# Performance work log

Hardware: AMD Instinct MI355X
Metric: run time of the kernel (lower is better)

The kernel has to match this reference:

```python
import jax, jax.numpy as jnp
import numpy as np

NUM_BUCKETS = 63  # clipped 1D relative positions: clip(j-i, -31, 31) + 31


def _rp_bucket(N):
    rel = jnp.arange(N)[None, :] - jnp.arange(N)[:, None]  # j - i
    half = NUM_BUCKETS // 2
    return (jnp.clip(rel, -half, half) + half).astype(jnp.int32)  # [N, N]


def setup_inputs() -> dict:
    key = jax.random.key(0)
    ks = jax.random.split(key, 7)
    B, N, C, H = 4, 1024, 1024, 16
    hd = C // H
    g = lambda k, shp, sc: jax.random.normal(k, shp, jnp.float32) * sc
    return {
        "x": g(ks[0], (B, N, C), 1.0),
        "w_qkv": g(ks[1], (3 * C, C), C ** -0.5),   # torch Linear weight [out, in]
        "w_proj": g(ks[2], (C, C), C ** -0.5),
        "b_proj": jnp.zeros((C,), jnp.float32),
        "rpe_q_table": g(ks[3], (H, hd, NUM_BUCKETS), 0.02),
        "rpe_k_table": g(ks[4], (H, hd, NUM_BUCKETS), 0.02),
        "rpe_v_table": g(ks[5], (H, NUM_BUCKETS, hd), 0.02),
    }


def reference(x, w_qkv, w_proj, b_proj, rpe_q_table, rpe_k_table, rpe_v_table):
    B, N, C = x.shape
    H = rpe_k_table.shape[0]
    hd = C // H
    scale = hd ** -0.5

    qkv = (x @ w_qkv.T).reshape(B, N, 3, H, hd).transpose(2, 0, 3, 1, 4)  # [3,B,H,N,hd]
    q, k, v = qkv[0] * scale, qkv[1], qkv[2]

    attn = jnp.einsum('bhid,bhjd->bhij', q, k)  # [B,H,N,N]

    rp = _rp_bucket(N)            # [N,N] int32 (static w.r.t. jit)
    idx = rp[None, None]          # [1,1,N,N]

    # rpe_k(q): contextual product, transposed=True -> bias added to scores
    qL = jnp.einsum('bhid,hdm->bhim', q, rpe_k_table)           # [B,H,N,nb]
    attn = attn + jnp.take_along_axis(qL, idx, axis=-1)

    # rpe_q(k * scale).transpose(2,3)
    kL = jnp.einsum('bhjd,hdm->bhjm', k * scale, rpe_q_table)   # [B,H,N,nb]
    attn = attn + jnp.swapaxes(jnp.take_along_axis(kL, idx, axis=-1), 2, 3)

    attn = jax.nn.softmax(attn, axis=-1)

    out = jnp.einsum('bhij,bhjd->bhid', attn, v)  # [B,H,N,hd]

    # rpe_v(attn): out[b,h,i,d] += sum_j attn[b,h,i,j] * Lv[h, rp[i,j], d]
    # segment-sum attn over buckets per query row, then contract with table.
    a_t = attn.transpose(2, 3, 0, 1)  # [Ni, Nj, B, H]
    S = jax.vmap(lambda a, seg: jax.ops.segment_sum(a, seg, num_segments=NUM_BUCKETS))(a_t, rp)  # [Ni,nb,B,H]
    out = out + jnp.einsum('inbh,hnd->bhid', S, rpe_v_table)

    x_out = out.transpose(0, 2, 1, 3).reshape(B, N, C)
    return x_out @ w_proj.T + b_proj
```

## Files before the change

### kernel.cpp

```cpp
#include <hip/hip_runtime.h>

typedef unsigned short u16;
typedef __attribute__((ext_vector_type(8))) short bf16x8;
typedef __attribute__((ext_vector_type(8))) unsigned short u16x8;
typedef __attribute__((ext_vector_type(4))) float f32x4;

#define MFMA16(a, b, c) __builtin_amdgcn_mfma_f32_16x16x32_bf16(a, b, c, 0, 0, 0)

__device__ __forceinline__ u16 f2bf(float f) {
  union { float f; unsigned u; } v; v.f = f;
  unsigned r = v.u + 0x7fffu + ((v.u >> 16) & 1u);
  return (u16)(r >> 16);
}
__device__ __forceinline__ float bf2f(u16 h) {
  union { unsigned u; float f; } v; v.u = ((unsigned)h) << 16;
  return v.f;
}
__device__ __forceinline__ void gl_lds16(const u16* g, u16* l) {
  __builtin_amdgcn_global_load_lds(
      (const __attribute__((address_space(1))) unsigned int*)g,
      (__attribute__((address_space(3))) unsigned int*)l, 16, 0, 0);
}

__global__ __launch_bounds__(256) void cvt_bf16_k(
    const float* __restrict__ x, const float* __restrict__ wq,
    const float* __restrict__ wp, u16* __restrict__ xb,
    u16* __restrict__ wqb, u16* __restrict__ wpb) {
  const size_t i = (size_t)blockIdx.x * 256 + threadIdx.x;
  const float* src; u16* dst; size_t off;
  if (i < 524288)       { src = x;  dst = xb;  off = i; }
  else if (i < 917504)  { src = wq; dst = wqb; off = i - 524288; }
  else                  { src = wp; dst = wpb; off = i - 917504; }
  const f32x4 a = ((const f32x4*)src)[off * 2];
  const f32x4 b = ((const f32x4*)src)[off * 2 + 1];
  u16x8 p;
#pragma unroll
  for (int e = 0; e < 4; ++e) { p[e] = f2bf(a[e]); p[e + 4] = f2bf(b[e]); }
  ((u16x8*)dst)[off] = p;
}

__global__ __launch_bounds__(256) void qkv_gemm_mfma(
    const u16* __restrict__ xb, const u16* __restrict__ wb,
    u16* __restrict__ qb, u16* __restrict__ kb, u16* __restrict__ vb) {
  __shared__ u16 At[128 * 64];
  __shared__ u16 Bt[128 * 64];
  const int tid = threadIdx.x;
  const int m0 = blockIdx.y * 128;
  const int o0 = blockIdx.x * 128;
  const int l = tid & 63, wv = tid >> 6;
  const int wm = (wv >> 1) * 64, wn = (wv & 1) * 64;
  const int lr = l & 15, lg = l >> 4;
  const int srow = l >> 3, scol = (l & 7) * 8;

  f32x4 acc[4][4];
#pragma unroll
  for (int i = 0; i < 4; ++i)
#pragma unroll
    for (int j = 0; j < 4; ++j) acc[i][j] = (f32x4){0.f, 0.f, 0.f, 0.f};

  for (int k0 = 0; k0 < 1024; k0 += 64) {
#pragma unroll
    for (int ii = 0; ii < 4; ++ii) {
      const int rbase = wv * 32 + ii * 8;
      gl_lds16(xb + (size_t)(m0 + rbase + srow) * 1024 + k0 + scol, At + rbase * 64);
      gl_lds16(wb + (size_t)(o0 + rbase + srow) * 1024 + k0 + scol, Bt + rbase * 64);
    }
    __syncthreads();
#pragma unroll
    for (int kg = 0; kg < 2; ++kg) {
      const int kbyte = (kg * 32 + 8 * lg) * 2;
      bf16x8 af[4], bfr[4];
#pragma unroll
      for (int mi = 0; mi < 4; ++mi)
        af[mi] = *(const bf16x8*)((const char*)At + (wm + mi * 16 + lr) * 128 + kbyte);
#pragma unroll
      for (int ni = 0; ni < 4; ++ni)
        bfr[ni] = *(const bf16x8*)((const char*)Bt + (wn + ni * 16 + lr) * 128 + kbyte);
#pragma unroll
      for (int mi = 0; mi < 4; ++mi)
#pragma unroll
        for (int ni = 0; ni < 4; ++ni)
          acc[mi][ni] = MFMA16(af[mi], bfr[ni], acc[mi][ni]);
    }
    __syncthreads();
  }

  const int o_base = o0 + wn;
  const int which = o_base >> 10;
  const int h = (o_base >> 6) & 15;
#pragma unroll
  for (int mi = 0; mi < 4; ++mi) {
#pragma unroll
    for (int ni = 0; ni < 4; ++ni) {
      const int d = ni * 16 + lr;
#pragma unroll
      for (int r = 0; r < 4; ++r) {
        int m = m0 + wm + mi * 16 + 4 * lg + r;
        int b_ = m >> 10, n_ = m & 1023;
        size_t dst = (((size_t)(b_ * 16 + h) * 1024) + n_) * 64 + d;
        float val = acc[mi][ni][r];
        if (which == 0)      qb[dst] = f2bf(val * 0.125f);
        else if (which == 1) kb[dst] = f2bf(val);
        else                 vb[dst] = f2bf(val);
      }
    }
  }
}

__global__ __launch_bounds__(256) void vtrans_k(const u16* __restrict__ vb,
                                                u16* __restrict__ vt) {
  __shared__ u16 ts[64][72];
  const int bh = blockIdx.x >> 4;
  const int nt = (blockIdx.x & 15) * 64;
  const int t = threadIdx.x;
#pragma unroll
  for (int i = 0; i < 2; ++i) {
    int c = t * 2 + i, n = c >> 3, c8 = (c & 7) * 8;
    *(u16x8*)&ts[n][c8] = *(const u16x8*)&vb[((size_t)bh * 1024 + nt + n) * 64 + c8];
  }
  __syncthreads();
#pragma unroll
  for (int i = 0; i < 2; ++i) {
    int c = t * 2 + i, d = c >> 3, n8 = (c & 7) * 8;
    u16x8 p;
#pragma unroll
    for (int j = 0; j < 8; ++j) p[j] = ts[n8 + j][d];
    *(u16x8*)&vt[((size_t)bh * 64 + d) * 1024 + nt + n8] = p;
  }
}

__global__ __launch_bounds__(256) void rpe_proj_k(
    const u16* __restrict__ q, const u16* __restrict__ k,
    const float* __restrict__ tq, const float* __restrict__ tk,
    u16* __restrict__ qL, u16* __restrict__ kL,
    u16* __restrict__ kL0, u16* __restrict__ kL62) {
  __shared__ float tqs[64 * 63], tks[64 * 63];
  __shared__ u16 qr[16 * 64], kr[16 * 64];
  const int tid = threadIdx.x;
  const int r0 = blockIdx.x * 16;
  const int h = (r0 >> 10) & 15;
  for (int i = tid; i < 1008; i += 256) {
    ((f32x4*)tqs)[i] = ((const f32x4*)(tq + (size_t)h * 4032))[i];
    ((f32x4*)tks)[i] = ((const f32x4*)(tk + (size_t)h * 4032))[i];
  }
  for (int i = tid; i < 128; i += 256) {
    ((u16x8*)qr)[i] = ((const u16x8*)(q + (size_t)r0 * 64))[i];
    ((u16x8*)kr)[i] = ((const u16x8*)(k + (size_t)r0 * 64))[i];
  }
  __syncthreads();
  const int wv = tid >> 6, t = tid & 63;
  if (t < 63) {
#pragma unroll
    for (int rr = 0; rr < 4; ++rr) {
      const int row = wv * 4 + rr;
      float aq = 0.f, ak = 0.f;
#pragma unroll 8
      for (int d = 0; d < 64; ++d) {
        aq += bf2f(qr[row * 64 + d]) * tks[d * 63 + t];
        ak += bf2f(kr[row * 64 + d]) * tqs[d * 63 + t];
      }
      ak *= 0.125f;
      qL[(size_t)(r0 + row) * 63 + t] = f2bf(aq);
      kL[(size_t)(r0 + row) * 63 + t] = f2bf(ak);
      if (t == 0)  kL0[r0 + row] = f2bf(ak);
      if (t == 62) kL62[r0 + row] = f2bf(ak);
    }
  }
}

__global__ __launch_bounds__(256, 3) void attn_mfma_k(
    const u16* __restrict__ qg, const u16* __restrict__ kgl,
    const u16* __restrict__ vtg, const u16* __restrict__ qLg,
    const u16* __restrict__ kLg, const u16* __restrict__ kL0g,
    const u16* __restrict__ kL62g, const float* __restrict__ tvg,
    u16* __restrict__ ao) {
  __shared__ u16 Kt[64 * 64];
  __shared__ u16 Vt[64 * 64];
  __shared__ u16 Pl[4 * 16 * 64];
  __shared__ u16 qLs[64 * 63];
  __shared__ u16 kLs[64 * 63];
  __shared__ u16 segs[64 * 63];
  __shared__ u16 kL0s[1024], kL62s[1024];
  __shared__ float rinv[64];

  const int tid = threadIdx.x;
  const int raw = blockIdx.x;
  const int bid = (raw & 7) * 128 + (raw >> 3);
  const int it = bid & 15;
  const int bh = bid >> 4;
  const int h = bh & 15;
  const int b_ = bh >> 4;
  const int i0 = it * 64;
  const int l = tid & 63, wv = tid >> 6;
  const int lr = l & 15, lg = l >> 4;
  const int iw0 = i0 + wv * 16;
  const size_t gbase = (size_t)bh * 1024;

  for (int i = tid; i < 504; i += 256) {
    ((u16x8*)segs)[i] = (u16x8){0, 0, 0, 0, 0, 0, 0, 0};
    ((u16x8*)qLs)[i] = ((const u16x8*)(qLg + (gbase + i0) * 63))[i];
  }
  for (int i = tid; i < 128; i += 256) {
    ((u16x8*)kL0s)[i] = ((const u16x8*)(kL0g + gbase))[i];
    ((u16x8*)kL62s)[i] = ((const u16x8*)(kL62g + gbase))[i];
  }
  bf16x8 qa[2];
  {
    const u16* qrow = qg + (gbase + iw0 + lr) * 64 + 8 * lg;
    qa[0] = *(const bf16x8*)(qrow);
    qa[1] = *(const bf16x8*)(qrow + 32);
  }
  const int cc0 = tid * 2;
  const int st_row0 = cc0 >> 3, st_chb0 = (cc0 & 7) * 16;
  const int st_row1 = (cc0 + 1) >> 3, st_chb1 = ((cc0 + 1) & 7) * 16;
  u16x8 Kr[2], Vr[2], kLr[2];
  {
    Kr[0] = *(const u16x8*)(kgl + (gbase + st_row0) * 64 + st_chb0 / 2);
    Kr[1] = *(const u16x8*)(kgl + (gbase + st_row1) * 64 + st_chb1 / 2);
    Vr[0] = *(const u16x8*)(vtg + ((size_t)bh * 64 + st_row0) * 1024 + st_chb0 / 2);
    Vr[1] = *(const u16x8*)(vtg + ((size_t)bh * 64 + st_row1) * 1024 + st_chb1 / 2);
    const bool band0 = (63 >= i0 - 31);
    if (band0 && tid < 252) {
      kLr[0] = ((const u16x8*)(kLg + gbase * 63))[tid * 2];
      kLr[1] = ((const u16x8*)(kLg + gbase * 63))[tid * 2 + 1];
    }
    const int d0 = st_row0 * 128 + (st_chb0 ^ ((st_row0 & 7) << 4));
    const int d1 = st_row1 * 128 + (st_chb1 ^ ((st_row1 & 7) << 4));
    *(u16x8*)((char*)Kt + d0) = Kr[0];
    *(u16x8*)((char*)Kt + d1) = Kr[1];
    *(u16x8*)((char*)Vt + d0) = Vr[0];
    *(u16x8*)((char*)Vt + d1) = Vr[1];
    if (band0 && tid < 252) {
      ((u16x8*)kLs)[tid * 2] = kLr[0];
      ((u16x8*)kLs)[tid * 2 + 1] = kLr[1];
    }
  }
  __syncthreads();

  float qL0r[4], qL62r[4];
#pragma unroll
  for (int r = 0; r < 4; ++r) {
    const int ir = wv * 16 + 4 * lg + r;
    qL0r[r] = bf2f(qLs[ir * 63 + 0]);
    qL62r[r] = bf2f(qLs[ir * 63 + 62]);
  }

  f32x4 pv[4];
#pragma unroll
  for (int db = 0; db < 4; ++db) pv[db] = (f32x4){0.f, 0.f, 0.f, 0.f};
  float lacc[4] = {0.f, 0.f, 0.f, 0.f}, racc[4] = {0.f, 0.f, 0.f, 0.f},
        rs[4] = {0.f, 0.f, 0.f, 0.f};

  for (int jt = 0; jt < 16; ++jt) {
    const int j0 = jt * 64;
    const int j0n = j0 + 64;
    const bool havenext = (jt < 15);
    const bool nband = havenext && (j0n + 63 >= i0 - 31) && (j0n <= i0 + 94);
    if (havenext) {
      Kr[0] = *(const u16x8*)(kgl + (gbase + j0n + st_row0) * 64 + st_chb0 / 2);
      Kr[1] = *(const u16x8*)(kgl + (gbase + j0n + st_row1) * 64 + st_chb1 / 2);
      Vr[0] = *(const u16x8*)(vtg + ((size_t)bh * 64 + st_row0) * 1024 + j0n + st_chb0 / 2);
      Vr[1] = *(const u16x8*)(vtg + ((size_t)bh * 64 + st_row1) * 1024 + j0n + st_chb1 / 2);
      if (nband && tid < 252) {
        kLr[0] = ((const u16x8*)(kLg + (gbase + j0n) * 63))[tid * 2];
        kLr[1] = ((const u16x8*)(kLg + (gbase + j0n) * 63))[tid * 2 + 1];
      }
    }

    const bool tband = (j0 + 63 >= i0 - 31) && (j0 <= i0 + 94);
#pragma unroll
    for (int cb = 0; cb < 4; ++cb) {
      f32x4 sc = (f32x4){0.f, 0.f, 0.f, 0.f};
#pragma unroll
      for (int kgi = 0; kgi < 2; ++kgi) {
        const int row = cb * 16 + lr;
        bf16x8 kf = *(const bf16x8*)((const char*)Kt + row * 128 +
                                     (((kgi * 32 + 8 * lg) * 2) ^ ((row & 7) << 4)));
        sc = MFMA16(qa[kgi], kf, sc);
      }
      const int jlo = j0 + cb * 16;
      const int jcol = jlo + lr;
      const int pcolb = (cb * 16 + lr) * 2;
      if (jlo + 15 <= iw0 - 31) {
        const float kl62 = bf2f(kL62s[jcol]);
#pragma unroll
        for (int r = 0; r < 4; ++r) {
          const float e = __expf(sc[r] + qL0r[r] + kl62);
          lacc[r] += e; rs[r] += e;
          const int prow = 4 * lg + r;
          *(u16*)((char*)Pl + wv * 2048 + prow * 128 + (pcolb ^ ((prow & 7) << 4))) = f2bf(e);
        }
      } else if (jlo >= iw0 + 46) {
        const float kl0 = bf2f(kL0s[jcol]);
#pragma unroll
        for (int r = 0; r < 4; ++r) {
          const float e = __expf(sc[r] + qL62r[r] + kl0);
          racc[r] += e; rs[r] += e;
          const int prow = 4 * lg + r;
          *(u16*)((char*)Pl + wv * 2048 + prow * 128 + (pcolb ^ ((prow & 7) << 4))) = f2bf(e);
        }
      } else {
#pragma unroll
        for (int r = 0; r < 4; ++r) {
          const int irow = iw0 + 4 * lg + r;
          int rel = jcol - irow;
          rel = rel < -31 ? -31 : (rel > 31 ? 31 : rel);
          const int m = rel + 31;
          const float bias = bf2f(qLs[(irow - i0) * 63 + m]) +
                             bf2f(kLs[(jcol - j0) * 63 + 62 - m]);
          const float e = __expf(sc[r] + bias);
          rs[r] += e;
          if (m == 0)       lacc[r] += e;
          else if (m == 62) racc[r] += e;
          else              segs[(irow - i0) * 63 + m] = f2bf(e);
          const int prow = 4 * lg + r;
          *(u16*)((char*)Pl + wv * 2048 + prow * 128 + (pcolb ^ ((prow & 7) << 4))) = f2bf(e);
        }
      }
    }
    (void)tband;
#pragma unroll
    for (int db = 0; db < 4; ++db) {
#pragma unroll
      for (int kgi = 0; kgi < 2; ++kgi) {
        bf16x8 pa = *(const bf16x8*)((const char*)Pl + wv * 2048 + lr * 128 +
                                     (((kgi * 32 + 8 * lg) * 2) ^ ((lr & 7) << 4)));
        const int vrow = db * 16 + lr;
        bf16x8 vf = *(const bf16x8*)((const char*)Vt + vrow * 128 +
                                     (((kgi * 32 + 8 * lg) * 2) ^ ((vrow & 7) << 4)));
        pv[db] = MFMA16(pa, vf, pv[db]);
      }
    }
    __syncthreads();
    if (havenext) {
      const int d0 = st_row0 * 128 + (st_chb0 ^ ((st_row0 & 7) << 4));
      const int d1 = st_row1 * 128 + (st_chb1 ^ ((st_row1 & 7) << 4));
      *(u16x8*)((char*)Kt + d0) = Kr[0];
      *(u16x8*)((char*)Kt + d1) = Kr[1];
      *(u16x8*)((char*)Vt + d0) = Vr[0];
      *(u16x8*)((char*)Vt + d1) = Vr[1];
      if (nband && tid < 252) {
        ((u16x8*)kLs)[tid * 2] = kLr[0];
        ((u16x8*)kLs)[tid * 2 + 1] = kLr[1];
      }
    }
    __syncthreads();
  }

#pragma unroll
  for (int r = 0; r < 4; ++r) {
#pragma unroll
    for (int m = 1; m < 16; m <<= 1) {
      rs[r] += __shfl_xor(rs[r], m);
      lacc[r] += __shfl_xor(lacc[r], m);
      racc[r] += __shfl_xor(racc[r], m);
    }
  }
  if (lr == 0) {
#pragma unroll
    for (int r = 0; r < 4; ++r) {
      const int ir = wv * 16 + 4 * lg + r;
      segs[ir * 63 + 0] = f2bf(lacc[r]);
      segs[ir * 63 + 62] = f2bf(racc[r]);
      rinv[ir] = 1.f / rs[r];
    }
  }
  __syncthreads();

#pragma unroll
  for (int db = 0; db < 4; ++db) {
    const int d = db * 16 + lr;
    float sadd[4] = {0.f, 0.f, 0.f, 0.f};
    for (int m = 0; m < 63; ++m) {
      const float tvv = tvg[((size_t)h * 63 + m) * 64 + d];
#pragma unroll
      for (int r = 0; r < 4; ++r)
        sadd[r] += bf2f(segs[(wv * 16 + 4 * lg + r) * 63 + m]) * tvv;
    }
#pragma unroll
    for (int r = 0; r < 4; ++r) {
      const int ir = wv * 16 + 4 * lg + r;
      const int irow = i0 + ir;
      const float val = (pv[db][r] + sadd[r]) * rinv[ir];
      ao[((size_t)(b_ * 1024) + irow) * 1024 + h * 64 + d] = f2bf(val);
    }
  }
}

__global__ __launch_bounds__(256) void proj_gemm_mfma(
    const u16* __restrict__ a, const u16* __restrict__ wpb,
    const float* __restrict__ bias, float* __restrict__ out) {
  __shared__ u16 At[128 * 64];
  __shared__ u16 Bt[128 * 64];
  const int tid = threadIdx.x;
  const int m0 = blockIdx.y * 128;
  const int o0 = blockIdx.x * 128;
  const int l = tid & 63, wv = tid >> 6;
  const int wm = (wv >> 1) * 64, wn = (wv & 1) * 64;
  const int lr = l & 15, lg = l >> 4;
  const int srow = l >> 3, scol = (l & 7) * 8;

  f32x4 acc[4][4];
#pragma unroll
  for (int i = 0; i < 4; ++i)
#pragma unroll
    for (int j = 0; j < 4; ++j) acc[i][j] = (f32x4){0.f, 0.f, 0.f, 0.f};

  for (int k0 = 0; k0 < 1024; k0 += 64) {
#pragma unroll
    for (int ii = 0; ii < 4; ++ii) {
      const int rbase = wv * 32 + ii * 8;
      gl_lds16(a + (size_t)(m0 + rbase + srow) * 1024 + k0 + scol, At + rbase * 64);
      gl_lds16(wpb + (size_t)(o0 + rbase + srow) * 1024 + k0 + scol, Bt + rbase * 64);
    }
    __syncthreads();
#pragma unroll
    for (int kg = 0; kg < 2; ++kg) {
      const int kbyte = (kg * 32 + 8 * lg) * 2;
      bf16x8 af[4], bfr[4];
#pragma unroll
      for (int mi = 0; mi < 4; ++mi)
        af[mi] = *(const bf16x8*)((const char*)At + (wm + mi * 16 + lr) * 128 + kbyte);
#pragma unroll
      for (int ni = 0; ni < 4; ++ni)
        bfr[ni] = *(const bf16x8*)((const char*)Bt + (wn + ni * 16 + lr) * 128 + kbyte);
#pragma unroll
      for (int mi = 0; mi < 4; ++mi)
#pragma unroll
        for (int ni = 0; ni < 4; ++ni)
          acc[mi][ni] = MFMA16(af[mi], bfr[ni], acc[mi][ni]);
    }
    __syncthreads();
  }
#pragma unroll
  for (int mi = 0; mi < 4; ++mi) {
#pragma unroll
    for (int ni = 0; ni < 4; ++ni) {
      const int o = o0 + wn + ni * 16 + lr;
      const float bv = bias[o];
#pragma unroll
      for (int r = 0; r < 4; ++r) {
        const int m = m0 + wm + mi * 16 + 4 * lg + r;
        out[(size_t)m * 1024 + o] = acc[mi][ni][r] + bv;
      }
    }
  }
}

extern "C" void kernel_launch(void* const* d_in, const int* in_sizes, int n_in,
                              void* d_out, int out_size, void* d_ws, size_t ws_size,
                              hipStream_t stream) {
  const float* x      = (const float*)d_in[0];
  const float* w_qkv  = (const float*)d_in[1];
  const float* w_proj = (const float*)d_in[2];
  const float* b_proj = (const float*)d_in[3];
  const float* tq     = (const float*)d_in[4];
  const float* tk     = (const float*)d_in[5];
  const float* tv     = (const float*)d_in[6];
  float* out = (float*)d_out;

  char* w8 = (char*)d_ws;
  u16* qb   = (u16*)(w8);
  u16* kb   = (u16*)(w8 + (8ull << 20));
  u16* vb   = (u16*)(w8 + (16ull << 20));
  u16* vt   = (u16*)(w8 + (24ull << 20));
  u16* aob  = (u16*)(w8 + (32ull << 20));
  u16* qL   = (u16*)(w8 + (40ull << 20));
  u16* kL   = (u16*)(w8 + (49ull << 20));
  u16* kL0  = (u16*)(w8 + (58ull << 20));
  u16* kL62 = (u16*)(w8 + (59ull << 20));
  u16* xb   = (u16*)(w8 + (60ull << 20));
  u16* wqb  = (u16*)(w8 + (68ull << 20));
  u16* wpb  = (u16*)(w8 + (74ull << 20));

  hipLaunchKernelGGL(cvt_bf16_k, dim3(4096), dim3(256), 0, stream,
                     x, w_qkv, w_proj, xb, wqb, wpb);
  hipLaunchKernelGGL(qkv_gemm_mfma, dim3(24, 32), dim3(256), 0, stream,
                     xb, wqb, qb, kb, vb);
  hipLaunchKernelGGL(vtrans_k, dim3(1024), dim3(256), 0, stream, vb, vt);
  hipLaunchKernelGGL(rpe_proj_k, dim3(4096), dim3(256), 0, stream,
                     qb, kb, tq, tk, qL, kL, kL0, kL62);
  hipLaunchKernelGGL(attn_mfma_k, dim3(1024), dim3(256), 0, stream,
                     qb, kb, vt, qL, kL, kL0, kL62, tv, aob);
  hipLaunchKernelGGL(proj_gemm_mfma, dim3(8, 32), dim3(256), 0, stream,
                     aob, wpb, b_proj, out);
}
```

Measured before the change: 325.8 us.

## Enlarge attention query tile to 128 rows with 512 threads sharing K/V tiles

The attention kernel now processes 128 query rows per block with 8 waves, so each staged K/V tile in shared memory is reused by twice as many query rows and the grid halves. The full per-head kL0/kL62 arrays are replaced by per-tile slices prefetched alongside K/V, which shrinks shared memory use. The band window for the kL prefetch is widened to match the taller tile. The QKV GEMM also gets a swizzled block order for better L2 locality. The trade-off is a larger block with heavier register and LDS pressure, and less parallelism per CU.

```diff
diff --git a/kernel.cpp b/kernel.cpp
--- a/kernel.cpp
+++ b/kernel.cpp
@@ -45,8 +45,10 @@
   __shared__ u16 At[128 * 64];
   __shared__ u16 Bt[128 * 64];
   const int tid = threadIdx.x;
-  const int m0 = blockIdx.y * 128;
-  const int o0 = blockIdx.x * 128;
+  const int lin = blockIdx.y * 24 + blockIdx.x;
+  const int swz = (lin & 7) * 96 + (lin >> 3);
+  const int m0 = (swz / 24) * 128;
+  const int o0 = (swz % 24) * 128;
   const int l = tid & 63, wv = tid >> 6;
   const int wm = (wv >> 1) * 64, wn = (wv & 1) * 64;
   const int lr = l & 15, lg = l >> 4;
@@ -168,7 +170,7 @@
   }
 }
 
-__global__ __launch_bounds__(256, 3) void attn_mfma_k(
+__global__ __launch_bounds__(512, 4) void attn_mfma_k(
     const u16* __restrict__ qg, const u16* __restrict__ kgl,
     const u16* __restrict__ vtg, const u16* __restrict__ qLg,
     const u16* __restrict__ kLg, const u16* __restrict__ kL0g,
@@ -176,33 +178,28 @@
     u16* __restrict__ ao) {
   __shared__ u16 Kt[64 * 64];
   __shared__ u16 Vt[64 * 64];
-  __shared__ u16 Pl[4 * 16 * 64];
-  __shared__ u16 qLs[64 * 63];
+  __shared__ u16 Pl[8 * 16 * 64];
+  __shared__ u16 qLs[128 * 63];
   __shared__ u16 kLs[64 * 63];
-  __shared__ u16 segs[64 * 63];
-  __shared__ u16 kL0s[1024], kL62s[1024];
-  __shared__ float rinv[64];
+  __shared__ u16 segs[128 * 63];
+  __shared__ u16 kl0t[64], kl62t[64];
 
   const int tid = threadIdx.x;
   const int raw = blockIdx.x;
-  const int bid = (raw & 7) * 128 + (raw >> 3);
-  const int it = bid & 15;
-  const int bh = bid >> 4;
+  const int bid = (raw & 7) * 64 + (raw >> 3);
+  const int it = bid & 7;
+  const int bh = bid >> 3;
   const int h = bh & 15;
   const int b_ = bh >> 4;
-  const int i0 = it * 64;
+  const int i0 = it * 128;
   const int l = tid & 63, wv = tid >> 6;
   const int lr = l & 15, lg = l >> 4;
   const int iw0 = i0 + wv * 16;
   const size_t gbase = (size_t)bh * 1024;
 
-  for (int i = tid; i < 504; i += 256) {
+  for (int i = tid; i < 1008; i += 512) {
     ((u16x8*)segs)[i] = (u16x8){0, 0, 0, 0, 0, 0, 0, 0};
     ((u16x8*)qLs)[i] = ((const u16x8*)(qLg + (gbase + i0) * 63))[i];
-  }
-  for (int i = tid; i < 128; i += 256) {
-    ((u16x8*)kL0s)[i] = ((const u16x8*)(kL0g + gbase))[i];
-    ((u16x8*)kL62s)[i] = ((const u16x8*)(kL62g + gbase))[i];
   }
   bf16x8 qa[2];
   {
@@ -210,30 +207,18 @@
     qa[0] = *(const bf16x8*)(qrow);
     qa[1] = *(const bf16x8*)(qrow + 32);
   }
-  const int cc0 = tid * 2;
-  const int st_row0 = cc0 >> 3, st_chb0 = (cc0 & 7) * 16;
-  const int st_row1 = (cc0 + 1) >> 3, st_chb1 = ((cc0 + 1) & 7) * 16;
-  u16x8 Kr[2], Vr[2], kLr[2];
+  const int st_row = tid >> 3, st_ch = tid & 7;
+  const int dstb = st_row * 128 + ((st_ch * 16) ^ ((st_row & 7) << 4));
+  u16x8 Kr, Vr, kLr, klr;
   {
-    Kr[0] = *(const u16x8*)(kgl + (gbase + st_row0) * 64 + st_chb0 / 2);
-    Kr[1] = *(const u16x8*)(kgl + (gbase + st_row1) * 64 + st_chb1 / 2);
-    Vr[0] = *(const u16x8*)(vtg + ((size_t)bh * 64 + st_row0) * 1024 + st_chb0 / 2);
-    Vr[1] = *(const u16x8*)(vtg + ((size_t)bh * 64 + st_row1) * 1024 + st_chb1 / 2);
-    const bool band0 = (63 >= i0 - 31);
-    if (band0 && tid < 252) {
-      kLr[0] = ((const u16x8*)(kLg + gbase * 63))[tid * 2];
-      kLr[1] = ((const u16x8*)(kLg + gbase * 63))[tid * 2 + 1];
-    }
-    const int d0 = st_row0 * 128 + (st_chb0 ^ ((st_row0 & 7) << 4));
-    const int d1 = st_row1 * 128 + (st_chb1 ^ ((st_row1 & 7) << 4));
-    *(u16x8*)((char*)Kt + d0) = Kr[0];
-    *(u16x8*)((char*)Kt + d1) = Kr[1];
-    *(u16x8*)((char*)Vt + d0) = Vr[0];
-    *(u16x8*)((char*)Vt + d1) = Vr[1];
-    if (band0 && tid < 252) {
-      ((u16x8*)kLs)[tid * 2] = kLr[0];
-      ((u16x8*)kLs)[tid * 2 + 1] = kLr[1];
-    }
+    Kr = *(const u16x8*)(kgl + (gbase + st_row) * 64 + st_ch * 8);
+    Vr = *(const u16x8*)(vtg + ((size_t)bh * 64 + st_row) * 1024 + st_ch * 8);
+    *(u16x8*)((char*)Kt + dstb) = Kr;
+    *(u16x8*)((char*)Vt + dstb) = Vr;
+    if (i0 == 0 && tid < 504)
+      ((u16x8*)kLs)[tid] = ((const u16x8*)(kLg + gbase * 63))[tid];
+    if (tid < 8)       ((u16x8*)kl0t)[tid] = ((const u16x8*)(kL0g + gbase))[tid];
+    else if (tid < 16) ((u16x8*)kl62t)[tid - 8] = ((const u16x8*)(kL62g + gbase))[tid - 8];
   }
   __syncthreads();
 
@@ -255,19 +240,16 @@
     const int j0 = jt * 64;
     const int j0n = j0 + 64;
     const bool havenext = (jt < 15);
-    const bool nband = havenext && (j0n + 63 >= i0 - 31) && (j0n <= i0 + 94);
+    const bool nband = havenext && (j0n >= i0 - 94) && (j0n <= i0 + 158);
     if (havenext) {
-      Kr[0] = *(const u16x8*)(kgl + (gbase + j0n + st_row0) * 64 + st_chb0 / 2);
-      Kr[1] = *(const u16x8*)(kgl + (gbase + j0n + st_row1) * 64 + st_chb1 / 2);
-      Vr[0] = *(const u16x8*)(vtg + ((size_t)bh * 64 + st_row0) * 1024 + j0n + st_chb0 / 2);
-      Vr[1] = *(const u16x8*)(vtg + ((size_t)bh * 64 + st_row1) * 1024 + j0n + st_chb1 / 2);
-      if (nband && tid < 252) {
-        kLr[0] = ((const u16x8*)(kLg + (gbase + j0n) * 63))[tid * 2];
-        kLr[1] = ((const u16x8*)(kLg + (gbase + j0n) * 63))[tid * 2 + 1];
-      }
-    }
-
-    const bool tband = (j0 + 63 >= i0 - 31) && (j0 <= i0 + 94);
+      Kr = *(const u16x8*)(kgl + (gbase + j0n + st_row) * 64 + st_ch * 8);
+      Vr = *(const u16x8*)(vtg + ((size_t)bh * 64 + st_row) * 1024 + j0n + st_ch * 8);
+      if (nband && tid < 504)
+        kLr = ((const u16x8*)(kLg + (gbase + j0n) * 63))[tid];
+      if (tid < 8)       klr = ((const u16x8*)(kL0g + gbase + j0n))[tid];
+      else if (tid < 16) klr = ((const u16x8*)(kL62g + gbase + j0n))[tid - 8];
+    }
+
 #pragma unroll
     for (int cb = 0; cb < 4; ++cb) {
       f32x4 sc = (f32x4){0.f, 0.f, 0.f, 0.f};
@@ -280,9 +262,10 @@
       }
       const int jlo = j0 + cb * 16;
       const int jcol = jlo + lr;
-      const int pcolb = (cb * 16 + lr) * 2;
+      const int jloc = cb * 16 + lr;
+      const int pcolb = jloc * 2;
       if (jlo + 15 <= iw0 - 31) {
-        const float kl62 = bf2f(kL62s[jcol]);
+        const float kl62 = bf2f(kl62t[jloc]);
 #pragma unroll
         for (int r = 0; r < 4; ++r) {
           const float e = __expf(sc[r] + qL0r[r] + kl62);
@@ -291,7 +274,7 @@
           *(u16*)((char*)Pl + wv * 2048 + prow * 128 + (pcolb ^ ((prow & 7) << 4))) = f2bf(e);
         }
       } else if (jlo >= iw0 + 46) {
-        const float kl0 = bf2f(kL0s[jcol]);
+        const float kl0 = bf2f(kl0t[jloc]);
 #pragma unroll
         for (int r = 0; r < 4; ++r) {
           const float e = __expf(sc[r] + qL62r[r] + kl0);
@@ -307,7 +290,7 @@
           rel = rel < -31 ? -31 : (rel > 31 ? 31 : rel);
           const int m = rel + 31;
           const float bias = bf2f(qLs[(irow - i0) * 63 + m]) +
-                             bf2f(kLs[(jcol - j0) * 63 + 62 - m]);
+                             bf2f(kLs[jloc * 63 + 62 - m]);
           const float e = __expf(sc[r] + bias);
           rs[r] += e;
           if (m == 0)       lacc[r] += e;
@@ -318,7 +301,6 @@
         }
       }
     }
-    (void)tband;
 #pragma unroll
     for (int db = 0; db < 4; ++db) {
 #pragma unroll
@@ -333,16 +315,11 @@
     }
     __syncthreads();
     if (havenext) {
-      const int d0 = st_row0 * 128 + (st_chb0 ^ ((st_row0 & 7) << 4));
-      const int d1 = st_row1 * 128 + (st_chb1 ^ ((st_row1 & 7) << 4));
-      *(u16x8*)((char*)Kt + d0) = Kr[0];
-      *(u16x8*)((char*)Kt + d1) = Kr[1];
-      *(u16x8*)((char*)Vt + d0) = Vr[0];
-      *(u16x8*)((char*)Vt + d1) = Vr[1];
-      if (nband && tid < 252) {
-        ((u16x8*)kLs)[tid * 2] = kLr[0];
-        ((u16x8*)kLs)[tid * 2 + 1] = kLr[1];
-      }
+      *(u16x8*)((char*)Kt + dstb) = Kr;
+      *(u16x8*)((char*)Vt + dstb) = Vr;
+      if (nband && tid < 504) ((u16x8*)kLs)[tid] = kLr;
+      if (tid < 8)       ((u16x8*)kl0t)[tid] = klr;
+      else if (tid < 16) ((u16x8*)kl62t)[tid - 8] = klr;
     }
     __syncthreads();
   }
@@ -362,7 +339,6 @@
       const int ir = wv * 16 + 4 * lg + r;
       segs[ir * 63 + 0] = f2bf(lacc[r]);
       segs[ir * 63 + 62] = f2bf(racc[r]);
-      rinv[ir] = 1.f / rs[r];
     }
   }
   __syncthreads();
@@ -379,9 +355,8 @@
     }
 #pragma unroll
     for (int r = 0; r < 4; ++r) {
-      const int ir = wv * 16 + 4 * lg + r;
-      const int irow = i0 + ir;
-      const float val = (pv[db][r] + sadd[r]) * rinv[ir];
+      const int irow = i0 + wv * 16 + 4 * lg + r;
+      const float val = (pv[db][r] + sadd[r]) / rs[r];
       ao[((size_t)(b_ * 1024) + irow) * 1024 + h * 64 + d] = f2bf(val);
     }
   }
@@ -480,7 +455,7 @@
   hipLaunchKernelGGL(vtrans_k, dim3(1024), dim3(256), 0, stream, vb, vt);
   hipLaunchKernelGGL(rpe_proj_k, dim3(4096), dim3(256), 0, stream,
                      qb, kb, tq, tk, qL, kL, kL0, kL62);
-  hipLaunchKernelGGL(attn_mfma_k, dim3(1024), dim3(256), 0, stream,
+  hipLaunchKernelGGL(attn_mfma_k, dim3(512), dim3(512), 0, stream,
                      qb, kb, vt, qL, kL, kL0, kL62, tv, aob);
   hipLaunchKernelGGL(proj_gemm_mfma, dim3(8, 32), dim3(256), 0, stream,
                      aob, wpb, b_proj, out);
```

New measurement: 328.9 us. Within noise of the previous version (+0.9%).
